# Optimization experiments

Hardware: AMD Instinct MI355X
Metric: run time of the kernel (lower is better)

## Reference

```python
import jax, jax.numpy as jnp
import numpy as np

B_SZ, SEQ, D_MODEL = 2, 512, 1024
EXPAND, HEAD_DIM = 2, 64
D_INNER = EXPAND * D_MODEL            # 2048
N_HEADS = D_INNER // HEAD_DIM         # 32
D_STATE = 64
EPS = 1e-6
PROJ_DIM = 2 * D_INNER + 2 * N_HEADS * D_STATE + N_HEADS  # 8224


def setup_inputs() -> dict:
    key = jax.random.key(0)
    k = jax.random.split(key, 5)
    return {
        "hidden": jax.random.normal(k[0], (B_SZ, SEQ, D_MODEL), jnp.float32),
        "W_in": 0.02 * jax.random.normal(k[1], (D_MODEL, PROJ_DIM), jnp.float32),
        "dt_bias": 0.5 * jax.random.normal(k[2], (N_HEADS,), jnp.float32),
        "A_log": 0.5 * jax.random.normal(k[3], (N_HEADS,), jnp.float32),
        "norm_weight": jnp.ones((D_INNER,), jnp.float32),
        "W_out": 0.02 * jax.random.normal(k[4], (D_INNER, D_MODEL), jnp.float32),
    }


def _rope(x, theta):
    # x: [b,l,h,n] interleaved pairs (view_as_complex convention); theta: [b,l,h,n//2]
    x0, x1 = x[..., 0::2], x[..., 1::2]
    c, s = jnp.cos(theta), jnp.sin(theta)
    y = jnp.stack([x0 * c - x1 * s, x0 * s + x1 * c], axis=-1)
    return y.reshape(x.shape)


def reference(hidden, W_in, dt_bias, A_log, norm_weight, W_out):
    b, l, _ = hidden.shape
    proj = hidden @ W_in  # [b,l,PROJ_DIM]
    hn = N_HEADS * D_STATE
    z = proj[..., :D_INNER]
    xr = proj[..., D_INNER:2 * D_INNER].reshape(b, l, N_HEADS, HEAD_DIM)
    Bm = proj[..., 2 * D_INNER:2 * D_INNER + hn].reshape(b, l, N_HEADS, D_STATE)
    Cm = proj[..., 2 * D_INNER + hn:2 * D_INNER + 2 * hn].reshape(b, l, N_HEADS, D_STATE)
    dt = jax.nn.softplus(proj[..., -N_HEADS:] + dt_bias)  # [b,l,h]

    A = -jnp.exp(A_log)                 # [h], negative decay
    alpha = jnp.exp(dt * A)             # decay factor
    beta = 0.5 * dt * alpha             # trapezoidal: half-step on previous input
    gamma = 0.5 * dt                    # trapezoidal: half-step on current input

    # data-dependent RoPE: phase is cumulative dt scaled by per-dim inverse freq
    half = D_STATE // 2
    inv_freq = 1.0 / (10000.0 ** (jnp.arange(half, dtype=jnp.float32) / half))
    theta = jnp.cumsum(dt, axis=1)[..., None] * inv_freq  # [b,l,h,half]
    Bm = _rope(Bm, theta)
    Cm = _rope(Cm, theta)

    # shifted (t-1) inputs, zero at t=0 (h starts at 0 so alpha-at-t0 is a no-op)
    Bp = jnp.pad(Bm[:, :-1], ((0, 0), (1, 0), (0, 0), (0, 0)))
    xp = jnp.pad(xr[:, :-1], ((0, 0), (1, 0), (0, 0), (0, 0)))

    tl = lambda t: jnp.moveaxis(t, 1, 0)  # time-major for scan
    xs = (tl(xr), tl(Bm), tl(Cm), tl(Bp), tl(xp), tl(alpha), tl(beta), tl(gamma))
    h0 = jnp.zeros((b, N_HEADS, D_STATE, HEAD_DIM), hidden.dtype)

    def step(h, inp):
        x_t, B_t, C_t, Bprev, xprev, a, bt, g = inp
        h = (a[..., None, None] * h
             + bt[..., None, None] * jnp.einsum('bhn,bhp->bhnp', Bprev, xprev)
             + g[..., None, None] * jnp.einsum('bhn,bhp->bhnp', B_t, x_t))
        y = jnp.einsum('bhn,bhnp->bhp', C_t, h)
        return h, y

    _, ys = jax.lax.scan(step, h0, xs)          # ys: [l,b,h,p]
    y = jnp.moveaxis(ys, 0, 1).reshape(b, l, D_INNER)

    y = y * jax.nn.silu(z)                      # gated output
    rms = jnp.sqrt(jnp.mean(y * y, axis=-1, keepdims=True) + EPS)
    y = y / rms * norm_weight                   # RMSNorm
    return y @ W_out
```

## Files before the change

kernel.cpp:

```cpp
#include <hip/hip_runtime.h>
#include <stdint.h>

typedef __attribute__((ext_vector_type(8))) short short8;
typedef __attribute__((ext_vector_type(8))) unsigned short ushort8;
typedef __attribute__((ext_vector_type(4))) unsigned short usv4;
typedef __attribute__((ext_vector_type(4))) float float4v;

#define B_SZ 2
#define SEQ 512
#define D_MODEL 1024
#define D_INNER 2048
#define N_HEADS 32
#define HEAD_DIM 64
#define D_STATE 64
#define PROJ_DIM 8224
#define NPAD 8320
#define MROWS 1024

__device__ __forceinline__ unsigned short f2bf(float f) {
    unsigned u = __builtin_bit_cast(unsigned, f);
    u += 0x7fffu + ((u >> 16) & 1u);
    return (unsigned short)(u >> 16);
}
__device__ __forceinline__ float bf2f(unsigned short h) {
    return __builtin_bit_cast(float, (unsigned)h << 16);
}

__device__ __forceinline__ void gld16(unsigned short* lds, const unsigned short* g) {
#if __has_builtin(__builtin_amdgcn_global_load_lds)
    __builtin_amdgcn_global_load_lds(
        (const __attribute__((address_space(1))) void*)g,
        (__attribute__((address_space(3))) void*)lds, 16, 0, 0);
#else
    *(short8*)lds = *(const short8*)g;
#endif
}

__device__ void transpose_body(const float* __restrict__ src,
                               unsigned short* __restrict__ dst,
                               int R, int C, int bx, int by, float* T, int tid) {
    int c0 = bx * 64, r0 = by * 64;
    int row = tid >> 2, cg = (tid & 3) * 16;
    #pragma unroll
    for (int k = 0; k < 4; k++) {
        int col = cg + k * 4;
        float4v v;
        if (c0 + col + 3 < C) {
            v = *(const float4v*)&src[(size_t)(r0 + row) * C + c0 + col];
        } else {
            #pragma unroll
            for (int e = 0; e < 4; e++)
                v[e] = (c0 + col + e < C) ? src[(size_t)(r0 + row) * C + c0 + col + e] : 0.f;
        }
        *(float4v*)&T[row * 68 + col] = v;
    }
    __syncthreads();
    int drow = tid >> 2, sg = (tid & 3) * 16;
    ushort8 v[2];
    #pragma unroll
    for (int k = 0; k < 16; k++) v[k >> 3][k & 7] = f2bf(T[(sg + k) * 68 + drow]);
    unsigned short* d = &dst[(size_t)(c0 + drow) * R + r0 + sg];
    *(ushort8*)&d[0] = v[0];
    *(ushort8*)&d[8] = v[1];
}

__global__ __launch_bounds__(256) void prep_fat(
    const float* __restrict__ hidden, const float* __restrict__ W_in,
    const float* __restrict__ W_out, unsigned short* __restrict__ Hb,
    unsigned short* __restrict__ Wt1, unsigned short* __restrict__ Wt2) {
    __shared__ float T[64 * 68];
    int blk = blockIdx.x, tid = threadIdx.x;
    if (blk < 1024) {
        int i = blk * 1024 + tid * 4;
        float4v v = *(const float4v*)&hidden[i];
        usv4 o;
        #pragma unroll
        for (int k = 0; k < 4; k++) o[k] = f2bf(v[k]);
        *(usv4*)&Hb[i] = o;
    } else if (blk < 3104) {
        int q = blk - 1024;
        transpose_body(W_in, Wt1, D_MODEL, PROJ_DIM, q % 130, q / 130, T, tid);
    } else {
        int q = blk - 3104;
        transpose_body(W_out, Wt2, D_INNER, D_MODEL, q % 16, q / 16, T, tid);
    }
}

template <bool BF16OUT>
__global__ __launch_bounds__(256) void gemm_bt(
    const unsigned short* __restrict__ A, const unsigned short* __restrict__ Bt,
    void* __restrict__ Cout, int M, int N, int K, int klen) {
    __shared__ unsigned short As[8192];
    __shared__ unsigned short Bs[8192];
    int tid = threadIdx.x;
    int lane = tid & 63, w = tid >> 6, quad = lane >> 4, l15 = lane & 15;
    int m0 = blockIdx.y * 128, n0 = blockIdx.x * 128;
    int kb = blockIdx.z * klen, ke = kb + klen;
    int wm = (w & 1) * 64, wn = (w >> 1) * 64;
    float4v acc[4][4];
    #pragma unroll
    for (int i = 0; i < 4; i++)
        #pragma unroll
        for (int j = 0; j < 4; j++) acc[i][j] = (float4v){0.f, 0.f, 0.f, 0.f};

    int rs = tid >> 3;
    int gl = ((tid & 7) ^ (rs & 7)) * 8;
    const unsigned short* ap = &A [(size_t)(m0 + rs) * K + gl];
    const unsigned short* bp = &Bt[(size_t)(n0 + rs) * K + gl];
    int rx = l15 & 7;

    for (int k0 = kb; k0 < ke; k0 += 64) {
        __syncthreads();
        #pragma unroll
        for (int p = 0; p < 4; p++) {
            gld16(&As[p * 2048 + tid * 8], ap + (size_t)(p * 32) * K + k0);
            gld16(&Bs[p * 2048 + tid * 8], bp + (size_t)(p * 32) * K + k0);
        }
        __syncthreads();
        #pragma unroll
        for (int kq = 0; kq < 2; kq++) {
            short8 af[4], bfr[4];
            #pragma unroll
            for (int mt = 0; mt < 4; mt++)
                af[mt] = *(const short8*)&As[(wm + mt * 16 + l15) * 64 + (((kq << 2) + quad) ^ rx) * 8];
            #pragma unroll
            for (int nt = 0; nt < 4; nt++)
                bfr[nt] = *(const short8*)&Bs[(wn + nt * 16 + l15) * 64 + (((kq << 2) + quad) ^ rx) * 8];
            #pragma unroll
            for (int mt = 0; mt < 4; mt++)
                #pragma unroll
                for (int nt = 0; nt < 4; nt++)
                    acc[mt][nt] = __builtin_amdgcn_mfma_f32_16x16x32_bf16(
                        af[mt], bfr[nt], acc[mt][nt], 0, 0, 0);
        }
    }
    #pragma unroll
    for (int mt = 0; mt < 4; mt++)
        #pragma unroll
        for (int nt = 0; nt < 4; nt++)
            #pragma unroll
            for (int r = 0; r < 4; r++) {
                int row = m0 + wm + mt * 16 + quad * 4 + r;
                int col = n0 + wn + nt * 16 + l15;
                if (col < N) {
                    if (BF16OUT)
                        ((unsigned short*)Cout)[(size_t)row * N + col] = f2bf(acc[mt][nt][r]);
                    else
                        ((float*)Cout)[(size_t)blockIdx.z * M * N + (size_t)row * N + col]
                            = acc[mt][nt][r];
                }
            }
}

__global__ __launch_bounds__(256) void reduce4(
    const float* __restrict__ P, float* __restrict__ out, int n) {
    int i = (blockIdx.x * 256 + threadIdx.x) * 4;
    float4v s = *(const float4v*)&P[i];
    #pragma unroll
    for (int z = 1; z < 4; z++) {
        float4v v = *(const float4v*)&P[(size_t)z * n + i];
        #pragma unroll
        for (int k = 0; k < 4; k++) s[k] += v[k];
    }
    *(float4v*)&out[i] = s;
}

__global__ __launch_bounds__(256) void dt_scan(
    const unsigned short* __restrict__ proj, const float* __restrict__ dt_bias,
    float* __restrict__ dt_arr, float* __restrict__ cum_arr) {
    __shared__ float chs[8];
    int bh = blockIdx.x;
    int b = bh >> 5, h = bh & 31;
    int tid = threadIdx.x, lane = tid & 63, w = tid >> 6;
    float bias = dt_bias[h];
    int t0 = w * 64 + lane, t1 = 256 + w * 64 + lane;
    float raw0 = bf2f(proj[(size_t)(b * SEQ + t0) * PROJ_DIM + 8192 + h]) + bias;
    float raw1 = bf2f(proj[(size_t)(b * SEQ + t1) * PROJ_DIM + 8192 + h]) + bias;
    float dt0 = raw0 > 20.f ? raw0 : log1pf(expf(raw0));
    float dt1 = raw1 > 20.f ? raw1 : log1pf(expf(raw1));
    float v0 = dt0, v1 = dt1;
    #pragma unroll
    for (int d = 1; d < 64; d <<= 1) {
        float n0 = __shfl_up(v0, d, 64);
        float n1 = __shfl_up(v1, d, 64);
        if (lane >= d) { v0 += n0; v1 += n1; }
    }
    if (lane == 63) { chs[w] = v0; chs[4 + w] = v1; }
    __syncthreads();
    float off0 = 0.f, off1 = 0.f;
    #pragma unroll
    for (int c = 0; c < 8; c++) {
        float s = chs[c];
        if (c < w) off0 += s;
        if (c < 4 + w) off1 += s;
    }
    dt_arr[bh * SEQ + t0] = dt0;  cum_arr[bh * SEQ + t0] = off0 + v0;
    dt_arr[bh * SEQ + t1] = dt1;  cum_arr[bh * SEQ + t1] = off1 + v1;
}

__global__ __launch_bounds__(256) void pack_fat(
    const unsigned short* __restrict__ proj, const float* __restrict__ cum_arr,
    unsigned short* __restrict__ Bh, unsigned short* __restrict__ Ch,
    unsigned short* __restrict__ Xt) {
    __shared__ unsigned short XT[64 * 72];
    int blk = blockIdx.x, tid = threadIdx.x;
    if (blk < 1024) {
        int m = blk, b = m >> 9, t = m & 511;
        const float k_l2 = 13.287712379549449f / 32.f;
        #pragma unroll
        for (int i = 0; i < 4; i++) {
            int q = i * 256 + tid;
            int h = q >> 5, j = q & 31;
            float cum = cum_arr[(b * 32 + h) * SEQ + t];
            float th = cum * exp2f(-(float)j * k_l2);
            float s, c;
            __sincosf(th, &s, &c);
            size_t rb = (size_t)m * PROJ_DIM;
            unsigned bu = *(const unsigned*)&proj[rb + 4096 + h * 64 + 2 * j];
            unsigned cu = *(const unsigned*)&proj[rb + 6144 + h * 64 + 2 * j];
            float b0 = bf2f((unsigned short)(bu & 0xffff)), b1 = bf2f((unsigned short)(bu >> 16));
            float c0 = bf2f((unsigned short)(cu & 0xffff)), c1 = bf2f((unsigned short)(cu >> 16));
            size_t dst = ((size_t)(b * 32 + h) * SEQ + t) * 64 + 2 * j;
            unsigned ob = (unsigned)f2bf(b0 * c - b1 * s) | ((unsigned)f2bf(b0 * s + b1 * c) << 16);
            unsigned oc = (unsigned)f2bf(c0 * c - c1 * s) | ((unsigned)f2bf(c0 * s + c1 * c) << 16);
            *(unsigned*)&Bh[dst] = ob;
            *(unsigned*)&Ch[dst] = oc;
        }
    } else {
        int q = blk - 1024;
        int bh = q >> 3, s0 = (q & 7) * 64;
        int b = bh >> 5, h = bh & 31;
        int r = tid >> 2, cg = (tid & 3) * 16;
        const unsigned short* src = &proj[(size_t)(b * SEQ + s0 + r) * PROJ_DIM + 2048 + h * 64 + cg];
        *(ushort8*)&XT[r * 72 + cg]     = *(const ushort8*)&src[0];
        *(ushort8*)&XT[r * 72 + cg + 8] = *(const ushort8*)&src[8];
        __syncthreads();
        int p = tid >> 2, sg = (tid & 3) * 16;
        ushort8 v[2];
        #pragma unroll
        for (int k = 0; k < 16; k++) v[k >> 3][k & 7] = XT[(sg + k) * 72 + p];
        unsigned short* dst = &Xt[((size_t)bh * 64 + p) * SEQ + s0 + sg];
        *(ushort8*)&dst[0] = v[0];
        *(ushort8*)&dst[8] = v[1];
    }
}

__global__ __launch_bounds__(256) void attn_tile(
    const unsigned short* __restrict__ Bh, const unsigned short* __restrict__ Ch,
    const unsigned short* __restrict__ Xt, const float* __restrict__ dt_arr,
    const float* __restrict__ cum_arr, const float* __restrict__ A_log,
    float* __restrict__ y_part) {
    __shared__ unsigned short Bs[4096];
    __shared__ unsigned short Xs[4096];
    __shared__ unsigned short Ps[4096];
    int pid = blockIdx.x;
    int qt = 0;
    while (pid >= ((qt + 2) >> 1)) { pid -= ((qt + 2) >> 1); qt++; }
    int slot = pid;
    int st0 = pid * 2;
    int nst = (st0 + 1 <= qt) ? 2 : 1;
    int bh = blockIdx.y;
    int b = bh >> 5, h = bh & 31;
    float Aneg = -expf(A_log[h]);
    int tid = threadIdx.x, lane = tid & 63, w = tid >> 6;
    int quad = lane >> 4, l15 = lane & 15;
    int rx = l15 & 7;

    int qrow = qt * 64 + w * 16 + l15;
    const unsigned short* Cptr = Ch + ((size_t)bh * SEQ + qrow) * 64;
    short8 cf[2];
    cf[0] = *(const short8*)&Cptr[quad * 8];
    cf[1] = *(const short8*)&Cptr[32 + quad * 8];

    int trow[4];
    float cumt[4];
    #pragma unroll
    for (int r = 0; r < 4; r++) {
        trow[r] = qt * 64 + w * 16 + quad * 4 + r;
        cumt[r] = cum_arr[bh * SEQ + trow[r]];
    }
    float4v yacc[4];
    #pragma unroll
    for (int i = 0; i < 4; i++) yacc[i] = (float4v){0.f, 0.f, 0.f, 0.f};

    int srow = tid >> 3, sg = tid & 7;
    int swz = (sg ^ (srow & 7)) * 8;

    for (int si = 0; si < nst; si++) {
        int st = st0 + si;
        __syncthreads();
        const unsigned short* bsrc = Bh + ((size_t)bh * SEQ + st * 64) * 64;
        gld16(&Bs[tid * 8],         bsrc + srow * 64 + swz);
        gld16(&Bs[(tid + 256) * 8], bsrc + (srow + 32) * 64 + swz);
        const unsigned short* xsrc = Xt + (size_t)bh * 64 * SEQ + st * 64;
        gld16(&Xs[tid * 8],         xsrc + (size_t)srow * SEQ + swz);
        gld16(&Xs[(tid + 256) * 8], xsrc + (size_t)(srow + 32) * SEQ + swz);
        __syncthreads();

        float4v sacc[4];
        #pragma unroll
        for (int i = 0; i < 4; i++) sacc[i] = (float4v){0.f, 0.f, 0.f, 0.f};
        #pragma unroll
        for (int kk = 0; kk < 2; kk++)
            #pragma unroll
            for (int nt = 0; nt < 4; nt++) {
                short8 bf8 = *(const short8*)&Bs[(nt * 16 + l15) * 64 + (((kk << 2) + quad) ^ rx) * 8];
                sacc[nt] = __builtin_amdgcn_mfma_f32_16x16x32_bf16(cf[kk], bf8, sacc[nt], 0, 0, 0);
            }
        #pragma unroll
        for (int nt = 0; nt < 4; nt++) {
            int s = st * 64 + nt * 16 + l15;
            float cums = cum_arr[bh * SEQ + s];
            float dts = dt_arr[bh * SEQ + s];
            float dts1 = (s + 1 < SEQ) ? dt_arr[bh * SEQ + s + 1] : 0.f;
            #pragma unroll
            for (int r = 0; r < 4; r++) {
                int t = trow[r];
                float wgt = (s > t) ? 0.f
                          : expf(Aneg * (cumt[r] - cums)) * 0.5f * (dts + ((s < t) ? dts1 : 0.f));
                int row = quad * 4 + r;
                int col = nt * 16 + l15;
                Ps[w * 1024 + row * 64 + (((col >> 3) ^ (row & 7)) << 3) + (col & 7)]
                    = f2bf(sacc[nt][r] * wgt);
            }
        }
        #pragma unroll
        for (int kk = 0; kk < 2; kk++) {
            short8 af = *(const short8*)&Ps[w * 1024 + l15 * 64 + (((kk << 2) + quad) ^ rx) * 8];
            #pragma unroll
            for (int pt = 0; pt < 4; pt++) {
                short8 xf = *(const short8*)&Xs[(pt * 16 + l15) * 64 + (((kk << 2) + quad) ^ rx) * 8];
                yacc[pt] = __builtin_amdgcn_mfma_f32_16x16x32_bf16(af, xf, yacc[pt], 0, 0, 0);
            }
        }
    }
    float* yp = y_part + (size_t)slot * ((size_t)MROWS * D_INNER);
    #pragma unroll
    for (int pt = 0; pt < 4; pt++)
        #pragma unroll
        for (int r = 0; r < 4; r++) {
            int t = trow[r];
            int p = pt * 16 + l15;
            yp[((size_t)b * SEQ + t) * D_INNER + h * 64 + p] = yacc[pt][r];
        }
}

__global__ __launch_bounds__(256) void gated_rmsnorm(
    const float* __restrict__ y_part, const unsigned short* __restrict__ proj,
    const float* __restrict__ nw, unsigned short* __restrict__ Y2) {
    __shared__ float red[4];
    int m = blockIdx.x, tid = threadIdx.x;
    int t = m & 511;
    int ns = ((t >> 6) + 2) >> 1;
    const unsigned short* zrow = proj + (size_t)m * PROJ_DIM;
    int j0 = tid * 8;
    float acc8[8];
    #pragma unroll
    for (int k = 0; k < 8; k++) acc8[k] = 0.f;
    for (int p = 0; p < ns; p++) {
        const float* yr = y_part + (size_t)p * ((size_t)MROWS * D_INNER) + (size_t)m * D_INNER + j0;
        float4v a = *(const float4v*)&yr[0];
        float4v c = *(const float4v*)&yr[4];
        acc8[0] += a[0]; acc8[1] += a[1]; acc8[2] += a[2]; acc8[3] += a[3];
        acc8[4] += c[0]; acc8[5] += c[1]; acc8[6] += c[2]; acc8[7] += c[3];
    }
    ushort8 zv = *(const ushort8*)&zrow[j0];
    float v[8];
    float ss = 0.f;
    #pragma unroll
    for (int k = 0; k < 8; k++) {
        float y = acc8[k];
        float z = bf2f(zv[k]);
        float g = y * (z / (1.f + expf(-z)));
        v[k] = g;
        ss += g * g;
    }
    #pragma unroll
    for (int d = 32; d > 0; d >>= 1) ss += __shfl_down(ss, d, 64);
    if ((tid & 63) == 0) red[tid >> 6] = ss;
    __syncthreads();
    float tot = red[0] + red[1] + red[2] + red[3];
    float inv = 1.0f / sqrtf(tot / (float)D_INNER + 1e-6f);
    #pragma unroll
    for (int k = 0; k < 8; k++)
        Y2[(size_t)m * D_INNER + j0 + k] = f2bf(v[k] * inv * nw[j0 + k]);
}


extern "C" void kernel_launch(void* const* d_in, const int* in_sizes, int n_in,
                              void* d_out, int out_size, void* d_ws, size_t ws_size,
                              hipStream_t stream) {
    const float* hidden   = (const float*)d_in[0];
    const float* W_in     = (const float*)d_in[1];
    const float* dt_bias  = (const float*)d_in[2];
    const float* A_log    = (const float*)d_in[3];
    const float* norm_w   = (const float*)d_in[4];
    const float* W_out    = (const float*)d_in[5];
    float* out = (float*)d_out;

    char* ws = (char*)d_ws;
    unsigned short* Wt1  = (unsigned short*)(ws);
    unsigned short* Hb   = (unsigned short*)(ws + 17039360);
    unsigned short* proj = (unsigned short*)(ws + 19136512);
    float* dt_arr        = (float*)(ws + 35979264);
    float* cum_arr       = (float*)(ws + 36110336);
    unsigned short* Bh   = (unsigned short*)(ws + 36241408);
    unsigned short* Ch   = (unsigned short*)(ws + 40435712);
    unsigned short* Xt   = (unsigned short*)(ws + 44630016);
    unsigned short* Y2   = (unsigned short*)(ws + 57212928);
    unsigned short* Wt2  = (unsigned short*)(ws + 61407232);
    float* y_part        = (float*)(ws + 65601536);
    float* Pk = (float*)proj;

    prep_fat<<<3616, 256, 0, stream>>>(hidden, W_in, W_out, Hb, Wt1, Wt2);
    gemm_bt<true><<<dim3(NPAD / 128, MROWS / 128, 1), 256, 0, stream>>>(
        Hb, Wt1, proj, MROWS, PROJ_DIM, D_MODEL, D_MODEL);
    dt_scan<<<64, 256, 0, stream>>>(proj, dt_bias, dt_arr, cum_arr);
    pack_fat<<<1536, 256, 0, stream>>>(proj, cum_arr, Bh, Ch, Xt);
    attn_tile<<<dim3(20, 64), 256, 0, stream>>>(Bh, Ch, Xt, dt_arr, cum_arr, A_log, y_part);
    gated_rmsnorm<<<MROWS, 256, 0, stream>>>(y_part, proj, norm_w, Y2);
    gemm_bt<false><<<dim3(D_MODEL / 128, MROWS / 128, 4), 256, 0, stream>>>(
        Y2, Wt2, Pk, MROWS, D_MODEL, D_INNER, D_INNER / 4);
    reduce4<<<MROWS * D_MODEL / 1024, 256, 0, stream>>>(Pk, out, MROWS * D_MODEL);
}
```

Before: 183.0 us.

## Double-buffer B/X tiles in attn_tile and widen source-tile groups to four

Each attention block now loops over up to four source tiles instead of two, which shrinks the grid and the number of partial y buffers that gated_rmsnorm must sum. B and X tiles are double-buffered in shared memory so the next tile's global loads are issued while the current tile is being computed. The aim is to hide load latency and cut partial-sum traffic, at the cost of more shared memory per block, fewer blocks, and a longer serial loop per block. The second-half swizzle also now uses the row index of the second half.

```diff
diff --git a/kernel.cpp b/kernel.cpp
--- a/kernel.cpp
+++ b/kernel.cpp
@@ -250,15 +250,15 @@
     const unsigned short* __restrict__ Xt, const float* __restrict__ dt_arr,
     const float* __restrict__ cum_arr, const float* __restrict__ A_log,
     float* __restrict__ y_part) {
-    __shared__ unsigned short Bs[4096];
-    __shared__ unsigned short Xs[4096];
+    __shared__ unsigned short Bs[2][4096];
+    __shared__ unsigned short Xs[2][4096];
     __shared__ unsigned short Ps[4096];
     int pid = blockIdx.x;
     int qt = 0;
-    while (pid >= ((qt + 2) >> 1)) { pid -= ((qt + 2) >> 1); qt++; }
+    while (pid >= ((qt + 4) >> 2)) { pid -= ((qt + 4) >> 2); qt++; }
     int slot = pid;
-    int st0 = pid * 2;
-    int nst = (st0 + 1 <= qt) ? 2 : 1;
+    int st0 = slot * 4;
+    int nst = qt - st0 + 1; if (nst > 4) nst = 4;
     int bh = blockIdx.y;
     int b = bh >> 5, h = bh & 31;
     float Aneg = -expf(A_log[h]);
@@ -266,6 +266,19 @@
     int quad = lane >> 4, l15 = lane & 15;
     int rx = l15 & 7;
 
+    int srow = tid >> 3, sg = tid & 7;
+    int swz = (sg ^ (srow & 7)) * 8;
+    int swz2 = (sg ^ ((srow + 32) & 7)) * 8;
+
+    {
+        const unsigned short* bsrc = Bh + ((size_t)bh * SEQ + st0 * 64) * 64;
+        gld16(&Bs[0][tid * 8],         bsrc + srow * 64 + swz);
+        gld16(&Bs[0][(tid + 256) * 8], bsrc + (srow + 32) * 64 + swz2);
+        const unsigned short* xsrc = Xt + (size_t)bh * 64 * SEQ + st0 * 64;
+        gld16(&Xs[0][tid * 8],         xsrc + (size_t)srow * SEQ + swz);
+        gld16(&Xs[0][(tid + 256) * 8], xsrc + (size_t)(srow + 32) * SEQ + swz2);
+    }
+
     int qrow = qt * 64 + w * 16 + l15;
     const unsigned short* Cptr = Ch + ((size_t)bh * SEQ + qrow) * 64;
     short8 cf[2];
@@ -283,19 +296,20 @@
     #pragma unroll
     for (int i = 0; i < 4; i++) yacc[i] = (float4v){0.f, 0.f, 0.f, 0.f};
 
-    int srow = tid >> 3, sg = tid & 7;
-    int swz = (sg ^ (srow & 7)) * 8;
-
     for (int si = 0; si < nst; si++) {
         int st = st0 + si;
+        int cur = si & 1;
         __syncthreads();
-        const unsigned short* bsrc = Bh + ((size_t)bh * SEQ + st * 64) * 64;
-        gld16(&Bs[tid * 8],         bsrc + srow * 64 + swz);
-        gld16(&Bs[(tid + 256) * 8], bsrc + (srow + 32) * 64 + swz);
-        const unsigned short* xsrc = Xt + (size_t)bh * 64 * SEQ + st * 64;
-        gld16(&Xs[tid * 8],         xsrc + (size_t)srow * SEQ + swz);
-        gld16(&Xs[(tid + 256) * 8], xsrc + (size_t)(srow + 32) * SEQ + swz);
-        __syncthreads();
+        if (si + 1 < nst) {
+            int nx = cur ^ 1;
+            int stn = st + 1;
+            const unsigned short* bsrc = Bh + ((size_t)bh * SEQ + stn * 64) * 64;
+            gld16(&Bs[nx][tid * 8],         bsrc + srow * 64 + swz);
+            gld16(&Bs[nx][(tid + 256) * 8], bsrc + (srow + 32) * 64 + swz2);
+            const unsigned short* xsrc = Xt + (size_t)bh * 64 * SEQ + stn * 64;
+            gld16(&Xs[nx][tid * 8],         xsrc + (size_t)srow * SEQ + swz);
+            gld16(&Xs[nx][(tid + 256) * 8], xsrc + (size_t)(srow + 32) * SEQ + swz2);
+        }
 
         float4v sacc[4];
         #pragma unroll
@@ -304,7 +318,7 @@
         for (int kk = 0; kk < 2; kk++)
             #pragma unroll
             for (int nt = 0; nt < 4; nt++) {
-                short8 bf8 = *(const short8*)&Bs[(nt * 16 + l15) * 64 + (((kk << 2) + quad) ^ rx) * 8];
+                short8 bf8 = *(const short8*)&Bs[cur][(nt * 16 + l15) * 64 + (((kk << 2) + quad) ^ rx) * 8];
                 sacc[nt] = __builtin_amdgcn_mfma_f32_16x16x32_bf16(cf[kk], bf8, sacc[nt], 0, 0, 0);
             }
         #pragma unroll
@@ -329,7 +343,7 @@
             short8 af = *(const short8*)&Ps[w * 1024 + l15 * 64 + (((kk << 2) + quad) ^ rx) * 8];
             #pragma unroll
             for (int pt = 0; pt < 4; pt++) {
-                short8 xf = *(const short8*)&Xs[(pt * 16 + l15) * 64 + (((kk << 2) + quad) ^ rx) * 8];
+                short8 xf = *(const short8*)&Xs[cur][(pt * 16 + l15) * 64 + (((kk << 2) + quad) ^ rx) * 8];
                 yacc[pt] = __builtin_amdgcn_mfma_f32_16x16x32_bf16(af, xf, yacc[pt], 0, 0, 0);
             }
         }
@@ -351,7 +365,7 @@
     __shared__ float red[4];
     int m = blockIdx.x, tid = threadIdx.x;
     int t = m & 511;
-    int ns = ((t >> 6) + 2) >> 1;
+    int ns = ((t >> 6) + 4) >> 2;
     const unsigned short* zrow = proj + (size_t)m * PROJ_DIM;
     int j0 = tid * 8;
     float acc8[8];
@@ -417,7 +431,7 @@
         Hb, Wt1, proj, MROWS, PROJ_DIM, D_MODEL, D_MODEL);
     dt_scan<<<64, 256, 0, stream>>>(proj, dt_bias, dt_arr, cum_arr);
     pack_fat<<<1536, 256, 0, stream>>>(proj, cum_arr, Bh, Ch, Xt);
-    attn_tile<<<dim3(20, 64), 256, 0, stream>>>(Bh, Ch, Xt, dt_arr, cum_arr, A_log, y_part);
+    attn_tile<<<dim3(12, 64), 256, 0, stream>>>(Bh, Ch, Xt, dt_arr, cum_arr, A_log, y_part);
     gated_rmsnorm<<<MROWS, 256, 0, stream>>>(y_part, proj, norm_w, Y2);
     gemm_bt<false><<<dim3(D_MODEL / 128, MROWS / 128, 4), 256, 0, stream>>>(
         Y2, Wt2, Pk, MROWS, D_MODEL, D_INNER, D_INNER / 4);
```

Result: no change. 182.4 us (-0.3%).
